# Kernel optimization log

Hardware: AMD Instinct MI355X
Metric: run time of the kernel (lower is better)

Reference implementation:

```python
import jax, jax.numpy as jnp
import numpy as np

B, T, D_MODEL, HEAD_DIM = 8, 2048, 1024, 128


def setup_inputs() -> dict:
    key = jax.random.key(0)
    k1, k2, k3, k4 = jax.random.split(key, 4)
    scale = 1.0 / np.sqrt(D_MODEL)
    return {
        "x": jax.random.normal(k1, (B, T, D_MODEL), dtype=jnp.float32),
        "Wq": jax.random.normal(k2, (HEAD_DIM, D_MODEL), dtype=jnp.float32) * scale,
        "Wk": jax.random.normal(k3, (HEAD_DIM, D_MODEL), dtype=jnp.float32) * scale,
        "Wv": jax.random.normal(k4, (HEAD_DIM, D_MODEL), dtype=jnp.float32) * scale,
    }


def reference(x, Wq, Wk, Wv) -> jnp.ndarray:
    # x: [B, T, C]; torch Linear(no bias): y = x @ W.T, W: [head_dim, d_model]
    q = jnp.einsum("btc,hc->bth", x, Wq)  # [B, T, H]
    k = jnp.einsum("btc,hc->bth", x, Wk)
    v = jnp.einsum("btc,hc->bth", x, Wv)
    head_dim = Wq.shape[0]
    scores = jnp.einsum("bqh,bkh->bqk", q, k) / jnp.sqrt(jnp.float32(head_dim))  # [B, T, T]
    T_ = x.shape[1]
    causal = jnp.tril(jnp.ones((T_, T_), dtype=bool))
    scores = jnp.where(causal, scores, -jnp.inf)
    probs = jax.nn.softmax(scores, axis=-1)
    # dropout is identity at inference (eval mode)
    out = jnp.einsum("bqk,bkh->bqh", probs, v)  # [B, T, head_dim]
    return out
```

## Files before the change

### kernel.cpp

```cpp
#include <hip/hip_runtime.h>
#include <hip/hip_bf16.h>
#include <math.h>

#define T_ 2048
#define C_ 1024
#define H_ 128
#define NB 8
#define WN 131072
#define SC 0.08838834764831845f

typedef __attribute__((ext_vector_type(8))) short bf16x8;
typedef __attribute__((ext_vector_type(8))) unsigned short u16x8;
typedef __attribute__((ext_vector_type(4))) float f32x4;

#define MFMA16(a,b,c) __builtin_amdgcn_mfma_f32_16x16x32_bf16((a),(b),(c),0,0,0)

__device__ __forceinline__ unsigned short f2bf(float f) {
    union { float f; unsigned u; } v; v.f = f;
    unsigned r = v.u + 0x7fffu + ((v.u >> 16) & 1u);
    return (unsigned short)(r >> 16);
}
__device__ __forceinline__ float bf2f(unsigned short u) {
    union { unsigned u; float f; } v; v.u = ((unsigned)u) << 16; return v.f;
}
__device__ __forceinline__ unsigned pk2bf(float a, float b) {
    __hip_bfloat162 h = __float22bfloat162_rn(float2{a, b});
    union { __hip_bfloat162 h; unsigned u; } v; v.h = h; return v.u;
}
__device__ __forceinline__ void gld16(void* lds, const void* g) {
    __builtin_amdgcn_global_load_lds(
        (const __attribute__((address_space(1))) unsigned*)g,
        (__attribute__((address_space(3))) unsigned*)lds, 16, 0, 0);
}

__global__ __launch_bounds__(256) void wconv(const float* __restrict__ Wq,
                                             const float* __restrict__ Wk,
                                             const float* __restrict__ Wv,
                                             unsigned short* __restrict__ Wb) {
    int e = (blockIdx.x * 256 + threadIdx.x) * 8;
    int which = e >> 17;
    int off = e & (WN - 1);
    const float* src = (which == 0) ? Wq : (which == 1 ? Wk : Wv);
    float s = (which == 0) ? SC : 1.0f;
    const float4* p = (const float4*)(src + off);
    float4 a = p[0], b = p[1];
    uint4 o = { pk2bf(a.x * s, a.y * s), pk2bf(a.z * s, a.w * s),
                pk2bf(b.x * s, b.y * s), pk2bf(b.z * s, b.w * s) };
    *(uint4*)(Wb + e) = o;
}

__global__ __launch_bounds__(256, 1) void proj(const float* __restrict__ x,
                                               const unsigned short* __restrict__ Wb,
                                               unsigned short* __restrict__ Q,
                                               unsigned short* __restrict__ K,
                                               unsigned short* __restrict__ V) {
    __shared__ unsigned short Xs[2][2][64][40];
    __shared__ unsigned short Ws[2][2][384][32];

    const int tid  = threadIdx.x;
    const int wave = tid >> 6, lane = tid & 63;
    const int quad = lane >> 4, l16 = lane & 15;
    const int m0   = blockIdx.x * 64;

    f32x4 acc[4][6];
    #pragma unroll
    for (int i = 0; i < 4; i++)
        #pragma unroll
        for (int j = 0; j < 6; j++) acc[i][j] = {0.f, 0.f, 0.f, 0.f};

    const int xrow = tid >> 2, xcg = tid & 3;
    const int xck = xcg >> 1, xco = (xcg & 1) * 16;
    const float* xg = x + (size_t)(m0 + xrow) * C_ + xcg * 16;
    const unsigned short* wg = Wb + (size_t)(wave * 96 + (lane >> 2)) * C_ + (lane & 3) * 8;

    #define STAGE(buf, kc) do {                                                   \
        _Pragma("unroll")                                                         \
        for (int kkc = 0; kkc < 2; kkc++)                                         \
            _Pragma("unroll")                                                     \
            for (int rb = 0; rb < 6; rb++)                                        \
                gld16(&Ws[buf][kkc][wave * 96 + rb * 16][0],                      \
                      wg + (size_t)rb * 16 * C_ + (kc) + kkc * 32);               \
        const float* xp = xg + (kc);                                              \
        float4 f0 = *(const float4*)xp,      f1 = *(const float4*)(xp + 4);       \
        float4 f2 = *(const float4*)(xp + 8), f3 = *(const float4*)(xp + 12);     \
        uint4 u0 = { pk2bf(f0.x,f0.y), pk2bf(f0.z,f0.w),                          \
                     pk2bf(f1.x,f1.y), pk2bf(f1.z,f1.w) };                        \
        uint4 u1 = { pk2bf(f2.x,f2.y), pk2bf(f2.z,f2.w),                          \
                     pk2bf(f3.x,f3.y), pk2bf(f3.z,f3.w) };                        \
        *(uint4*)&Xs[buf][xck][xrow][xco]     = u0;                               \
        *(uint4*)&Xs[buf][xck][xrow][xco + 8] = u1;                               \
    } while (0)

    STAGE(0, 0);
    for (int it = 0; it < 16; it++) {
        __syncthreads();
        if (it < 15) { STAGE((it + 1) & 1, (it + 1) * 64); }
        const int buf = it & 1;
        bf16x8 af[4][2];
        #pragma unroll
        for (int kk = 0; kk < 2; kk++)
            #pragma unroll
            for (int mf = 0; mf < 4; mf++)
                af[mf][kk] = *(bf16x8*)&Xs[buf][kk][mf * 16 + l16][quad * 8];
        #pragma unroll
        for (int kk = 0; kk < 2; kk++)
            #pragma unroll
            for (int nf = 0; nf < 6; nf++) {
                bf16x8 bq = *(bf16x8*)&Ws[buf][kk][wave * 96 + nf * 16 + l16][quad * 8];
                #pragma unroll
                for (int mf = 0; mf < 4; mf++)
                    acc[mf][nf] = MFMA16(af[mf][kk], bq, acc[mf][nf]);
            }
    }
    #undef STAGE

    #pragma unroll
    for (int nf = 0; nf < 6; nf++) {
        int nb = wave * 96 + nf * 16;
        int which = nb >> 7;
        unsigned short* dst = (which == 0) ? Q : (which == 1 ? K : V);
        int c = (nb & 127) + l16;
        #pragma unroll
        for (int mf = 0; mf < 4; mf++)
            #pragma unroll
            for (int r = 0; r < 4; r++)
                dst[(size_t)(m0 + mf * 16 + quad * 4 + r) * H_ + c] = f2bf(acc[mf][nf][r]);
    }
}

__global__ __launch_bounds__(256, 3) void attn(const unsigned short* __restrict__ Qg,
                                               const unsigned short* __restrict__ Kg,
                                               const unsigned short* __restrict__ Vg,
                                               unsigned short* __restrict__ Ob,
                                               float* __restrict__ Ml) {
    const int bx = blockIdx.x;
    const int s  = bx & 7, qt = 31 - (bx >> 3);
    const int b  = blockIdx.y;
    const int qbase = qt * 64, kstart = s * 256;
    if (kstart > qbase) return;
    const int kend  = (kstart + 256 < qbase + 64) ? kstart + 256 : qbase + 64;
    const int niter = (kend - kstart) >> 6;

    __shared__ unsigned short Ks[4][64][32];
    __shared__ unsigned short Vt[128 * 64];
    __shared__ unsigned short Ps[4][16][64];

    const int tid = threadIdx.x, wave = tid >> 6, lane = tid & 63;
    const int quad = lane >> 4, l16 = lane & 15;
    const size_t base = (size_t)b * T_ * H_;

    const unsigned short* ksrc = Kg + base + (size_t)(kstart + (lane >> 2)) * H_ + wave * 32 + (lane & 3) * 8;
    #pragma unroll
    for (int p = 0; p < 4; p++) gld16(&Ks[wave][p * 16][0], ksrc + (size_t)p * 16 * H_);
    const unsigned short* vsrc = Vg + base + (size_t)(kstart + wave * 8 + quad * 2) * H_ + l16 * 8;
    u16x8 vr[2][2];
    vr[0][0] = *(const u16x8*)vsrc;             vr[0][1] = *(const u16x8*)(vsrc + H_);
    vr[1][0] = *(const u16x8*)(vsrc + 32 * H_); vr[1][1] = *(const u16x8*)(vsrc + 33 * H_);

    bf16x8 qf[4];
    const unsigned short* qp = Qg + base + (size_t)(qbase + wave * 16 + l16) * H_ + quad * 8;
    #pragma unroll
    for (int kk = 0; kk < 4; kk++) qf[kk] = *(const bf16x8*)(qp + kk * 32);

    f32x4 o[8];
    #pragma unroll
    for (int i = 0; i < 8; i++) o[i] = {0.f, 0.f, 0.f, 0.f};
    float m_i = -INFINITY, l_i = 0.f;
    const int swz = (l16 & 7) << 3;
    const int qg = qbase + wave * 16 + l16;

    __syncthreads();

    #pragma unroll
    for (int g = 0; g < 2; g++) {
        int t0 = wave * 8 + g * 32 + quad * 2;
        int t8 = t0 >> 3;
        #pragma unroll
        for (int j = 0; j < 8; j++) {
            int h = l16 * 8 + j;
            unsigned pk = (unsigned)(unsigned short)vr[g][0][j] | ((unsigned)(unsigned short)vr[g][1][j] << 16);
            int blk = (t8 ^ (h & 7) ^ ((h >> 3) & 7)) & 7;
            *(unsigned*)&Vt[h * 64 + blk * 8 + (t0 & 7)] = pk;
        }
    }

    for (int kt = 0; ; kt++) {
        const int kbase = kstart + kt * 64;
        f32x4 st[4];
        #pragma unroll
        for (int nf = 0; nf < 4; nf++) st[nf] = {0.f, 0.f, 0.f, 0.f};
        #pragma unroll
        for (int kk = 0; kk < 4; kk++)
            #pragma unroll
            for (int nf = 0; nf < 4; nf++) {
                bf16x8 kfr = *(bf16x8*)&Ks[kk][nf * 16 + l16][quad * 8];
                st[nf] = MFMA16(kfr, qf[kk], st[nf]);
            }
        if (kbase + 64 > qbase) {
            #pragma unroll
            for (int nf = 0; nf < 4; nf++) {
                int kg = kbase + nf * 16 + quad * 4;
                #pragma unroll
                for (int r = 0; r < 4; r++)
                    if (kg + r > qg) st[nf][r] = -INFINITY;
            }
        }
        float mx = st[0][0];
        #pragma unroll
        for (int nf = 0; nf < 4; nf++)
            #pragma unroll
            for (int r = 0; r < 4; r++) mx = fmaxf(mx, st[nf][r]);
        mx = fmaxf(mx, __shfl_xor(mx, 16, 64));
        mx = fmaxf(mx, __shfl_xor(mx, 32, 64));
        float mnew = fmaxf(m_i, mx);
        float al = __expf(m_i - mnew);
        m_i = mnew;
        float rs = 0.f;
        #pragma unroll
        for (int nf = 0; nf < 4; nf++)
            #pragma unroll
            for (int r = 0; r < 4; r++) {
                float e = __expf(st[nf][r] - mnew);
                st[nf][r] = e; rs += e;
            }
        rs += __shfl_xor(rs, 16, 64);
        rs += __shfl_xor(rs, 32, 64);
        l_i = al * l_i + rs;
        #pragma unroll
        for (int nf = 0; nf < 4; nf++) {
            uint2 pk = { pk2bf(st[nf][0], st[nf][1]), pk2bf(st[nf][2], st[nf][3]) };
            *(uint2*)&Ps[wave][l16][(nf * 16 + quad * 4) ^ swz] = pk;
        }
        float a0 = __shfl(al, quad * 4 + 0, 64), a1 = __shfl(al, quad * 4 + 1, 64);
        float a2 = __shfl(al, quad * 4 + 2, 64), a3 = __shfl(al, quad * 4 + 3, 64);
        #pragma unroll
        for (int i = 0; i < 8; i++) {
            o[i][0] *= a0; o[i][1] *= a1; o[i][2] *= a2; o[i][3] *= a3;
        }
        __syncthreads();

        const bool more = (kt + 1 < niter);
        if (more) {
            ksrc += 64 * H_;
            #pragma unroll
            for (int p = 0; p < 4; p++) gld16(&Ks[wave][p * 16][0], ksrc + (size_t)p * 16 * H_);
            vsrc += 64 * H_;
            vr[0][0] = *(const u16x8*)vsrc;             vr[0][1] = *(const u16x8*)(vsrc + H_);
            vr[1][0] = *(const u16x8*)(vsrc + 32 * H_); vr[1][1] = *(const u16x8*)(vsrc + 33 * H_);
        }
        bf16x8 pa0 = *(bf16x8*)&Ps[wave][l16][(quad * 8) ^ swz];
        bf16x8 pa1 = *(bf16x8*)&Ps[wave][l16][(32 + quad * 8) ^ swz];
        #pragma unroll
        for (int nf = 0; nf < 8; nf++) {
            int h = nf * 16 + l16;
            int ex = (h & 7) ^ ((h >> 3) & 7);
            bf16x8 v0 = *(bf16x8*)&Vt[h * 64 + ((quad ^ ex) & 7) * 8];
            bf16x8 v1 = *(bf16x8*)&Vt[h * 64 + (((quad + 4) ^ ex) & 7) * 8];
            o[nf] = MFMA16(pa0, v0, o[nf]);
            o[nf] = MFMA16(pa1, v1, o[nf]);
        }
        if (!more) break;
        __syncthreads();
        #pragma unroll
        for (int g = 0; g < 2; g++) {
            int t0 = wave * 8 + g * 32 + quad * 2;
            int t8 = t0 >> 3;
            #pragma unroll
            for (int j = 0; j < 8; j++) {
                int h = l16 * 8 + j;
                unsigned pk = (unsigned)(unsigned short)vr[g][0][j] | ((unsigned)(unsigned short)vr[g][1][j] << 16);
                int blk = (t8 ^ (h & 7) ^ ((h >> 3) & 7)) & 7;
                *(unsigned*)&Vt[h * 64 + blk * 8 + (t0 & 7)] = pk;
            }
        }
    }

    const int g2 = qt >> 2;
    const int Pq = 2 * g2 * (g2 + 1) + (qt & 3) * (g2 + 1);
    const int slot = (Pq + s) * NB + b;
    float lq[4];
    #pragma unroll
    for (int r = 0; r < 4; r++) lq[r] = __shfl(l_i, quad * 4 + r, 64);
    const size_t obase = (size_t)slot * 64 * 128;
    #pragma unroll
    for (int r = 0; r < 4; r++) {
        float invl = 1.0f / lq[r];
        #pragma unroll
        for (int nf = 0; nf < 8; nf++)
            Ob[obase + (size_t)(wave * 16 + quad * 4 + r) * 128 + nf * 16 + l16] = f2bf(o[nf][r] * invl);
    }
    if (lane < 16) {
        int ridx = slot * 64 + wave * 16 + l16;
        Ml[ridx * 2]     = m_i;
        Ml[ridx * 2 + 1] = l_i;
    }
}

__global__ __launch_bounds__(256) void merge(const unsigned short* __restrict__ Ob,
                                             const float* __restrict__ Ml,
                                             float* __restrict__ out) {
    const int qt = blockIdx.x, b = blockIdx.y;
    const int g = qt >> 2;
    const int Pq = 2 * g * (g + 1) + (qt & 3) * (g + 1);
    const int ns = g + 1;
    const int tid = threadIdx.x;
    const int row = tid >> 2, c0 = (tid & 3) * 32;

    float mv[8], lv[8], mg = -INFINITY;
    for (int s2 = 0; s2 < ns; s2++) {
        int slot = (Pq + s2) * NB + b;
        mv[s2] = Ml[(slot * 64 + row) * 2];
        lv[s2] = Ml[(slot * 64 + row) * 2 + 1];
        mg = fmaxf(mg, mv[s2]);
    }
    float L = 0.f, w[8];
    for (int s2 = 0; s2 < ns; s2++) { w[s2] = lv[s2] * __expf(mv[s2] - mg); L += w[s2]; }
    float inv = 1.0f / L;

    float accv[32];
    #pragma unroll
    for (int i = 0; i < 32; i++) accv[i] = 0.f;
    for (int s2 = 0; s2 < ns; s2++) {
        int slot = (Pq + s2) * NB + b;
        const unsigned short* op = Ob + ((size_t)(slot * 64 + row)) * 128 + c0;
        #pragma unroll
        for (int cc = 0; cc < 4; cc++) {
            u16x8 v = *(const u16x8*)(op + cc * 8);
            #pragma unroll
            for (int j = 0; j < 8; j++) accv[cc * 8 + j] += w[s2] * bf2f(v[j]);
        }
    }
    float* od = out + ((size_t)(b * T_ + qt * 64 + row)) * 128 + c0;
    #pragma unroll
    for (int cc = 0; cc < 8; cc++) {
        float4 w4 = { accv[cc*4] * inv, accv[cc*4+1] * inv, accv[cc*4+2] * inv, accv[cc*4+3] * inv };
        *(float4*)(od + cc * 4) = w4;
    }
}

extern "C" void kernel_launch(void* const* d_in, const int* in_sizes, int n_in,
                              void* d_out, int out_size, void* d_ws, size_t ws_size,
                              hipStream_t stream) {
    const float* x  = (const float*)d_in[0];
    const float* Wq = (const float*)d_in[1];
    const float* Wk = (const float*)d_in[2];
    const float* Wv = (const float*)d_in[3];

    char* ws = (char*)d_ws;
    unsigned short* Wb = (unsigned short*)ws;
    unsigned short* Q  = (unsigned short*)(ws + (size_t) 1 * (1u << 20));
    unsigned short* K  = (unsigned short*)(ws + (size_t) 5 * (1u << 20));
    unsigned short* V  = (unsigned short*)(ws + (size_t) 9 * (1u << 20));
    unsigned short* Ob = (unsigned short*)(ws + (size_t)13 * (1u << 20));
    float*          Ml = (float*)(ws + (size_t)32 * (1u << 20));
    float* out = (float*)d_out;

    hipLaunchKernelGGL(wconv, dim3(192), dim3(256), 0, stream, Wq, Wk, Wv, Wb);
    hipLaunchKernelGGL(proj,  dim3(256), dim3(256), 0, stream, x, Wb, Q, K, V);
    hipLaunchKernelGGL(attn,  dim3(256, NB), dim3(256), 0, stream, Q, K, V, Ob, Ml);
    hipLaunchKernelGGL(merge, dim3(32, NB), dim3(256), 0, stream, Ob, Ml, out);
}
```

Measured before the change: 173.8 us.

## Drop LDS staging in projection GEMM, load fragments directly from global memory

Rewrites the QKV projection kernel to skip shared-memory double buffering. Each wave now loads its x and weight MFMA fragments straight from global memory, with 32-row tiles and twice as many blocks. This removes LDS traffic and __syncthreads barriers and raises occupancy, at the cost of less reuse: each of the 4 waves re-reads and re-converts the same x rows, and the per-lane strided 16-byte global loads may coalesce poorly.

```diff
diff --git a/kernel.cpp b/kernel.cpp
--- a/kernel.cpp
+++ b/kernel.cpp
@@ -49,70 +49,44 @@
     *(uint4*)(Wb + e) = o;
 }
 
-__global__ __launch_bounds__(256, 1) void proj(const float* __restrict__ x,
-                                               const unsigned short* __restrict__ Wb,
-                                               unsigned short* __restrict__ Q,
-                                               unsigned short* __restrict__ K,
-                                               unsigned short* __restrict__ V) {
-    __shared__ unsigned short Xs[2][2][64][40];
-    __shared__ unsigned short Ws[2][2][384][32];
-
+__global__ __launch_bounds__(256) void proj(const float* __restrict__ x,
+                                            const unsigned short* __restrict__ Wb,
+                                            unsigned short* __restrict__ Q,
+                                            unsigned short* __restrict__ K,
+                                            unsigned short* __restrict__ V) {
     const int tid  = threadIdx.x;
     const int wave = tid >> 6, lane = tid & 63;
     const int quad = lane >> 4, l16 = lane & 15;
-    const int m0   = blockIdx.x * 64;
-
-    f32x4 acc[4][6];
-    #pragma unroll
-    for (int i = 0; i < 4; i++)
+    const int m0   = blockIdx.x * 32;
+
+    f32x4 acc[2][6];
+    #pragma unroll
+    for (int i = 0; i < 2; i++)
         #pragma unroll
         for (int j = 0; j < 6; j++) acc[i][j] = {0.f, 0.f, 0.f, 0.f};
 
-    const int xrow = tid >> 2, xcg = tid & 3;
-    const int xck = xcg >> 1, xco = (xcg & 1) * 16;
-    const float* xg = x + (size_t)(m0 + xrow) * C_ + xcg * 16;
-    const unsigned short* wg = Wb + (size_t)(wave * 96 + (lane >> 2)) * C_ + (lane & 3) * 8;
-
-    #define STAGE(buf, kc) do {                                                   \
-        _Pragma("unroll")                                                         \
-        for (int kkc = 0; kkc < 2; kkc++)                                         \
-            _Pragma("unroll")                                                     \
-            for (int rb = 0; rb < 6; rb++)                                        \
-                gld16(&Ws[buf][kkc][wave * 96 + rb * 16][0],                      \
-                      wg + (size_t)rb * 16 * C_ + (kc) + kkc * 32);               \
-        const float* xp = xg + (kc);                                              \
-        float4 f0 = *(const float4*)xp,      f1 = *(const float4*)(xp + 4);       \
-        float4 f2 = *(const float4*)(xp + 8), f3 = *(const float4*)(xp + 12);     \
-        uint4 u0 = { pk2bf(f0.x,f0.y), pk2bf(f0.z,f0.w),                          \
-                     pk2bf(f1.x,f1.y), pk2bf(f1.z,f1.w) };                        \
-        uint4 u1 = { pk2bf(f2.x,f2.y), pk2bf(f2.z,f2.w),                          \
-                     pk2bf(f3.x,f3.y), pk2bf(f3.z,f3.w) };                        \
-        *(uint4*)&Xs[buf][xck][xrow][xco]     = u0;                               \
-        *(uint4*)&Xs[buf][xck][xrow][xco + 8] = u1;                               \
-    } while (0)
-
-    STAGE(0, 0);
-    for (int it = 0; it < 16; it++) {
-        __syncthreads();
-        if (it < 15) { STAGE((it + 1) & 1, (it + 1) * 64); }
-        const int buf = it & 1;
-        bf16x8 af[4][2];
-        #pragma unroll
-        for (int kk = 0; kk < 2; kk++)
-            #pragma unroll
-            for (int mf = 0; mf < 4; mf++)
-                af[mf][kk] = *(bf16x8*)&Xs[buf][kk][mf * 16 + l16][quad * 8];
-        #pragma unroll
-        for (int kk = 0; kk < 2; kk++)
-            #pragma unroll
-            for (int nf = 0; nf < 6; nf++) {
-                bf16x8 bq = *(bf16x8*)&Ws[buf][kk][wave * 96 + nf * 16 + l16][quad * 8];
-                #pragma unroll
-                for (int mf = 0; mf < 4; mf++)
-                    acc[mf][nf] = MFMA16(af[mf][kk], bq, acc[mf][nf]);
-            }
-    }
-    #undef STAGE
+    const float* xp0 = x + (size_t)(m0 + l16) * C_ + quad * 8;
+    const float* xp1 = x + (size_t)(m0 + 16 + l16) * C_ + quad * 8;
+    const unsigned short* wp = Wb + (size_t)(wave * 96 + l16) * C_ + quad * 8;
+
+    #pragma unroll 2
+    for (int ko = 0; ko < C_; ko += 32) {
+        float4 a00 = *(const float4*)(xp0 + ko);
+        float4 a01 = *(const float4*)(xp0 + ko + 4);
+        float4 a10 = *(const float4*)(xp1 + ko);
+        float4 a11 = *(const float4*)(xp1 + ko + 4);
+        union { uint4 u; bf16x8 h; } af0, af1;
+        af0.u = uint4{ pk2bf(a00.x, a00.y), pk2bf(a00.z, a00.w),
+                       pk2bf(a01.x, a01.y), pk2bf(a01.z, a01.w) };
+        af1.u = uint4{ pk2bf(a10.x, a10.y), pk2bf(a10.z, a10.w),
+                       pk2bf(a11.x, a11.y), pk2bf(a11.z, a11.w) };
+        #pragma unroll
+        for (int nf = 0; nf < 6; nf++) {
+            bf16x8 bw = *(const bf16x8*)(wp + (size_t)nf * 16 * C_ + ko);
+            acc[0][nf] = MFMA16(af0.h, bw, acc[0][nf]);
+            acc[1][nf] = MFMA16(af1.h, bw, acc[1][nf]);
+        }
+    }
 
     #pragma unroll
     for (int nf = 0; nf < 6; nf++) {
@@ -121,7 +95,7 @@
         unsigned short* dst = (which == 0) ? Q : (which == 1 ? K : V);
         int c = (nb & 127) + l16;
         #pragma unroll
-        for (int mf = 0; mf < 4; mf++)
+        for (int mf = 0; mf < 2; mf++)
             #pragma unroll
             for (int r = 0; r < 4; r++)
                 dst[(size_t)(m0 + mf * 16 + quad * 4 + r) * H_ + c] = f2bf(acc[mf][nf][r]);
@@ -356,7 +330,7 @@
     float* out = (float*)d_out;
 
     hipLaunchKernelGGL(wconv, dim3(192), dim3(256), 0, stream, Wq, Wk, Wv, Wb);
-    hipLaunchKernelGGL(proj,  dim3(256), dim3(256), 0, stream, x, Wb, Q, K, V);
+    hipLaunchKernelGGL(proj,  dim3(512), dim3(256), 0, stream, x, Wb, Q, K, V);
     hipLaunchKernelGGL(attn,  dim3(256, NB), dim3(256), 0, stream, Q, K, V, Ob, Ml);
     hipLaunchKernelGGL(merge, dim3(32, NB), dim3(256), 0, stream, Ob, Ml, out);
 }
```

Result: slower. 218.4 us (+25.6%).
